# Optimization experiments

Hardware: AMD Instinct MI355X
Metric: run time of the kernel (lower is better)

The kernel has to match this reference:

```python
import jax, jax.numpy as jnp
import numpy as np

D_MODEL = 1024
NUM_HEADS = 16
HEAD_DIM = D_MODEL // NUM_HEADS
LN_EPS = 1e-3  # Keras LayerNormalization default epsilon


def setup_inputs() -> dict:
    key = jax.random.key(0)
    ks = jax.random.split(key, 7)
    s = 1.0 / np.sqrt(D_MODEL)
    return {
        "x": jax.random.normal(ks[0], (2, 2048, D_MODEL), dtype=jnp.float32),
        "Wq": jax.random.normal(ks[1], (D_MODEL, D_MODEL), dtype=jnp.float32) * s,
        "bq": jnp.zeros((D_MODEL,), dtype=jnp.float32),
        "Wk": jax.random.normal(ks[2], (D_MODEL, D_MODEL), dtype=jnp.float32) * s,
        "bk": jnp.zeros((D_MODEL,), dtype=jnp.float32),
        "Wv": jax.random.normal(ks[3], (D_MODEL, D_MODEL), dtype=jnp.float32) * s,
        "bv": jnp.zeros((D_MODEL,), dtype=jnp.float32),
        "ln_gamma": jnp.ones((D_MODEL,), dtype=jnp.float32),
        "ln_beta": jnp.zeros((D_MODEL,), dtype=jnp.float32),
    }


def _split_heads(t):
    # [B, S, D] -> [B, H, S, Dh]; matches tf.split(axis=2)+concat(axis=0) math
    B, S, D = t.shape
    return t.reshape(B, S, NUM_HEADS, HEAD_DIM).transpose(0, 2, 1, 3)


def reference(x, Wq, bq, Wk, bk, Wv, bv, ln_gamma, ln_beta):
    Q = _split_heads(x @ Wq + bq)   # [B,H,S,Dh]
    K = _split_heads(x @ Wk + bk)
    V = _split_heads(x @ Wv + bv)
    scale = 1.0 / jnp.sqrt(jnp.asarray(HEAD_DIM, dtype=x.dtype))
    scores = jnp.einsum("bhqd,bhkd->bhqk", Q, K) * scale
    probs = jax.nn.softmax(scores, axis=-1)  # dropout is identity at inference
    ctx = jnp.einsum("bhqk,bhkd->bhqd", probs, V)
    out = ctx.transpose(0, 2, 1, 3).reshape(x.shape)  # merge heads -> [B,S,D]
    out = out + x  # residual
    mean = jnp.mean(out, axis=-1, keepdims=True)
    var = jnp.mean(jnp.square(out - mean), axis=-1, keepdims=True)
    return (out - mean) * jax.lax.rsqrt(var + LN_EPS) * ln_gamma + ln_beta
```

## Files before the change

### kernel.cpp

```cpp
#include <hip/hip_runtime.h>
#include <stdint.h>

#define D_MODEL 1024
#define SEQ     2048
#define BATCH   2
#define NHEADS  16
#define HDIM    64
#define ROWS    (BATCH*SEQ)

typedef __attribute__((ext_vector_type(8)))  short short8;
typedef __attribute__((ext_vector_type(4)))  float f32x4;
typedef __attribute__((ext_vector_type(16))) float f32x16;
typedef __attribute__((ext_vector_type(4)))  short short4v;

__device__ __forceinline__ unsigned short f2bf(float f){
  union { float f; unsigned int u; } v; v.f = f;
  unsigned int r = v.u + 0x7fffu + ((v.u >> 16) & 1u);
  return (unsigned short)(r >> 16);
}

__device__ __forceinline__ float fast_exp2(float x){
  float r;
  asm("v_exp_f32 %0, %1" : "=v"(r) : "v"(x));
  return r;
}

__device__ __forceinline__ float f3(float a, float b, float c){
  return fmaxf(fmaxf(a,b),c);
}

__device__ __forceinline__ void gload16(const void* g, void* l){
  __builtin_amdgcn_global_load_lds((__attribute__((address_space(1))) void*)(uintptr_t)g,
                                   (__attribute__((address_space(3))) void*)l, 16, 0, 0);
}

__global__ __launch_bounds__(256) void prep(const float* __restrict__ x,
                                            const float* __restrict__ Wq,
                                            const float* __restrict__ Wk,
                                            const float* __restrict__ Wv,
                                            unsigned short* __restrict__ xb,
                                            unsigned short* __restrict__ Wt){
  __shared__ float tile[32][33];
  const int bidx = blockIdx.x;
  if (bidx < 4096){
    const int i = bidx*256 + threadIdx.x;
    float4 v = ((const float4*)x)[i];
    short4v o;
    o[0] = (short)f2bf(v.x); o[1] = (short)f2bf(v.y);
    o[2] = (short)f2bf(v.z); o[3] = (short)f2bf(v.w);
    ((short4v*)xb)[i] = o;
  } else {
    const int wz  = bidx - 4096;
    const int mat = wz >> 10;
    const int idx = wz & 1023;
    const float* W = (mat==0)?Wq:((mat==1)?Wk:Wv);
    unsigned short* dst = Wt + (size_t)mat*1048576;
    const int tx = threadIdx.x & 31, ty = threadIdx.x >> 5;
    const int n0 = (idx & 31)*32, k0 = (idx >> 5)*32;
    #pragma unroll
    for (int j=0;j<32;j+=8)
      tile[ty+j][tx] = W[(size_t)(k0+ty+j)*D_MODEL + n0+tx];
    __syncthreads();
    #pragma unroll
    for (int j=0;j<32;j+=8)
      dst[(size_t)(n0+ty+j)*D_MODEL + k0+tx] = f2bf(tile[tx][ty+j]);
  }
}

__global__ __launch_bounds__(256) void qkv_gemm(
    const unsigned short* __restrict__ xb, const unsigned short* __restrict__ wtb,
    const float* __restrict__ bq, const float* __restrict__ bk, const float* __restrict__ bv,
    unsigned short* __restrict__ qb, unsigned short* __restrict__ kbuf,
    unsigned short* __restrict__ vbuf)
{
  __shared__ unsigned short As[128*32];
  __shared__ unsigned short Bs[128*32];
  const int mat = blockIdx.z;
  const unsigned short* wt = wtb + (size_t)mat*1048576;
  const float* bias = (mat==0)?bq:((mat==1)?bk:bv);
  unsigned short* outp = (mat==0)?qb:((mat==1)?kbuf:vbuf);
  const float osc = (mat==0)?0.18033688011112042f:1.0f;
  const int bm = blockIdx.x, bn = blockIdx.y;
  const int t = threadIdx.x, w = t>>6, lane = t&63;
  const int g = lane>>4, l15 = lane&15;
  const int wm = w>>1, wn = w&1;

  const int srow = (w<<5) + (lane>>2);
  const int scol = (lane&3)*8;

  f32x4 acc[4][4];
  #pragma unroll
  for (int i=0;i<4;++i)
    #pragma unroll
    for (int j=0;j<4;++j) acc[i][j] = (f32x4){0.f,0.f,0.f,0.f};

  for (int kt=0; kt<32; ++kt){
    const int k0 = kt*32;
    #pragma unroll
    for (int j=0;j<2;++j){
      gload16(xb + (size_t)(bm*128 + srow + j*16)*D_MODEL + k0 + scol, &As[(w<<10)+(j<<9)]);
      gload16(wt + (size_t)(bn*128 + srow + j*16)*D_MODEL + k0 + scol, &Bs[(w<<10)+(j<<9)]);
    }
    __syncthreads();
    short8 a[4], b[4];
    #pragma unroll
    for (int mr=0;mr<4;++mr) a[mr] = *(const short8*)&As[(wm*64 + mr*16 + l15)*32 + g*8];
    #pragma unroll
    for (int nr=0;nr<4;++nr) b[nr] = *(const short8*)&Bs[(wn*64 + nr*16 + l15)*32 + g*8];
    #pragma unroll
    for (int mr=0;mr<4;++mr)
      #pragma unroll
      for (int nr=0;nr<4;++nr)
        acc[mr][nr] = __builtin_amdgcn_mfma_f32_16x16x32_bf16(a[mr], b[nr], acc[mr][nr], 0,0,0);
    __syncthreads();
  }
  #pragma unroll
  for (int mr=0;mr<4;++mr){
    const int rowb = bm*128 + wm*64 + mr*16 + g*4;
    #pragma unroll
    for (int nr=0;nr<4;++nr){
      const int col = bn*128 + wn*64 + nr*16 + l15;
      const float bsv = bias[col];
      const int h = col>>6, d = col&63;
      #pragma unroll
      for (int r=0;r<4;++r){
        const int m = rowb + r;
        const int b_ = m>>11, s = m&2047;
        outp[(((size_t)(b_*NHEADS + h))*SEQ + s)*HDIM + d] = f2bf((acc[mr][nr][r] + bsv)*osc);
      }
    }
  }
}

__global__ __launch_bounds__(256) void vtrans(const unsigned short* __restrict__ vb,
                                              unsigned short* __restrict__ vt){
  __shared__ unsigned short tile[64*72];
  const int bh = blockIdx.y;
  const int s0 = blockIdx.x*64;
  const int t = threadIdx.x;
  {
    const int s_loc = t>>2, d0 = (t&3)*16;
    const unsigned short* src = vb + ((size_t)bh*SEQ + s0 + s_loc)*HDIM + d0;
    *(short8*)&tile[s_loc*72 + d0]     = *(const short8*)src;
    *(short8*)&tile[s_loc*72 + d0 + 8] = *(const short8*)(src+8);
  }
  __syncthreads();
  {
    const int d = t>>2, sc = (t&3)*16;
    short8 o0, o1;
    #pragma unroll
    for (int j=0;j<8;++j){
      o0[j] = (short)tile[(sc+j)*72 + d];
      o1[j] = (short)tile[(sc+8+j)*72 + d];
    }
    unsigned short* dst = vt + ((size_t)bh*HDIM + d)*SEQ + s0 + sc;
    *(short8*)dst     = o0;
    *(short8*)(dst+8) = o1;
  }
}

__global__ __launch_bounds__(256, 2) void attn_fwd(
  const unsigned short* __restrict__ Qb, const unsigned short* __restrict__ Kb,
  const unsigned short* __restrict__ Vtb, float* __restrict__ ctx)
{
  __shared__ unsigned short Ks[4][4096];
  __shared__ unsigned short Vs[4][4096];
  const int lin = blockIdx.x;
  const int bh = (lin&7)*4 + (lin>>7);
  const int q0 = ((lin>>3)&15)*128;
  const int t = threadIdx.x, w = t>>6, lane = t&63;
  const int l31 = lane&31, hi = lane>>5;
  const unsigned short* Qh  = Qb  + (size_t)bh*SEQ*HDIM;
  const unsigned short* Kh  = Kb  + (size_t)bh*SEQ*HDIM;
  const unsigned short* Vth = Vtb + (size_t)bh*HDIM*SEQ;

  const int qrow = q0 + w*32 + l31;
  short8 qf[4];
  #pragma unroll
  for (int dht=0;dht<4;++dht)
    qf[dht] = *(const short8*)&Qh[(size_t)qrow*HDIM + dht*16 + hi*8];

  const int srow0 = t>>3,        srow1 = (256+t)>>3;
  const int skk0  = ((t&7)<<3) ^ ((srow0&7)<<3);
  const int skk1  = ((t&7)<<3) ^ ((srow1&7)<<3);
  const int rx    = l31&7;

  float m = 0.f;
  float rsum = 0.f;
  f32x16 o0, o1;
  #pragma unroll
  for (int r=0;r<16;++r){ o0[r]=0.f; o1[r]=0.f; }

#define STAGE(buf, ktile) do {                                                    \
    const int kb_ = (ktile)*64;                                                   \
    gload16(&Kh[(size_t)(kb_ + srow0)*HDIM + skk0], &Ks[buf][(w*64)*8]);          \
    gload16(&Kh[(size_t)(kb_ + srow1)*HDIM + skk1], &Ks[buf][(256 + w*64)*8]);    \
    gload16(&Vth[(size_t)srow0*SEQ + kb_ + skk0],   &Vs[buf][(w*64)*8]);          \
    gload16(&Vth[(size_t)srow1*SEQ + kb_ + skk1],   &Vs[buf][(256 + w*64)*8]);    \
  } while(0)

#define BODY(CUR, KT, HASST, WAITN, FIRST) do {                                   \
    if ((WAITN)==4) asm volatile("s_waitcnt vmcnt(4)" ::: "memory");              \
    else            asm volatile("s_waitcnt vmcnt(0)" ::: "memory");              \
    __builtin_amdgcn_s_barrier();                                                 \
    __builtin_amdgcn_sched_barrier(0);                                            \
    if (HASST) STAGE(((CUR)+2)&3, (KT)+2);                                        \
                                       \
    f32x16 s0, s1;                                                                \
    _Pragma("unroll")                                                             \
    for (int r=0;r<16;++r){ s0[r]=0.f; s1[r]=0.f; }                               \
    __builtin_amdgcn_s_setprio(1);                                                \
    _Pragma("unroll")                                                             \
    for (int dht=0;dht<4;++dht){                                                  \
      short8 kf = *(const short8*)&Ks[CUR][l31*64 + (((dht<<1)|hi) ^ rx)*8];      \
      s0 = __builtin_amdgcn_mfma_f32_32x32x16_bf16(kf, qf[dht], s0, 0,0,0);       \
    }                                                                             \
    _Pragma("unroll")                                                             \
    for (int dht=0;dht<4;++dht){                                                  \
      short8 kf = *(const short8*)&Ks[CUR][(32+l31)*64 + (((dht<<1)|hi) ^ rx)*8]; \
      s1 = __builtin_amdgcn_mfma_f32_32x32x16_bf16(kf, qf[dht], s1, 0,0,0);       \
    }                                                                             \
    __builtin_amdgcn_s_setprio(0);                                                \
    if (FIRST){                                                                   \
      float a0=f3(s0[0],s0[1],s0[2]),  a1=f3(s0[3],s0[4],s0[5]);                  \
      float a2=f3(s0[6],s0[7],s0[8]),  a3=f3(s0[9],s0[10],s0[11]);                \
      float a4=f3(s0[12],s0[13],s0[14]), a5=f3(s0[15],s1[0],s1[1]);               \
      float a6=f3(s1[2],s1[3],s1[4]),  a7=f3(s1[5],s1[6],s1[7]);                  \
      float a8=f3(s1[8],s1[9],s1[10]), a9=f3(s1[11],s1[12],s1[13]);               \
      float a10=fmaxf(s1[14],s1[15]);                                             \
      float rmx = f3(f3(a0,a1,a2), f3(a3,a4,a5), f3(f3(a6,a7,a8), a9, a10));      \
      m = fmaxf(rmx, __shfl_xor(rmx, 32));                                        \
    }                                                                             \
          \
    unsigned int u[8], vv[8];                                                     \
    _Pragma("unroll")                                                             \
    for (int i=0;i<8;++i){                                                        \
      float e0 = fast_exp2(s0[2*i]   - m);                                        \
      float e1 = fast_exp2(s0[2*i+1] - m);                                        \
      float e2 = fast_exp2(s1[2*i]   - m);                                        \
      float e3 = fast_exp2(s1[2*i+1] - m);                                        \
      rsum += (e0+e1)+(e2+e3);                                                    \
      asm("v_cvt_pk_bf16_f32 %0, %1, %2" : "=v"(u[i])  : "v"(e0), "v"(e1));       \
      asm("v_cvt_pk_bf16_f32 %0, %1, %2" : "=v"(vv[i]) : "v"(e2), "v"(e3));       \
    }                                                                             \
    asm("v_permlane32_swap_b32 %0, %1" : "+v"(u[0]),  "+v"(u[2]));                \
    asm("v_permlane32_swap_b32 %0, %1" : "+v"(u[1]),  "+v"(u[3]));                \
    asm("v_permlane32_swap_b32 %0, %1" : "+v"(u[4]),  "+v"(u[6]));                \
    asm("v_permlane32_swap_b32 %0, %1" : "+v"(u[5]),  "+v"(u[7]));                \
    asm("v_permlane32_swap_b32 %0, %1" : "+v"(vv[0]), "+v"(vv[2]));               \
    asm("v_permlane32_swap_b32 %0, %1" : "+v"(vv[1]), "+v"(vv[3]));               \
    asm("v_permlane32_swap_b32 %0, %1" : "+v"(vv[4]), "+v"(vv[6]));               \
    asm("v_permlane32_swap_b32 %0, %1" : "+v"(vv[5]), "+v"(vv[7]));               \
    union U8 { unsigned int wq[4]; short8 s; };                                   \
    short8 pa[4];                                                                 \
    { U8 x; x.wq[0]=u[0];  x.wq[1]=u[1];  x.wq[2]=u[2];  x.wq[3]=u[3];  pa[0]=x.s; } \
    { U8 x; x.wq[0]=u[4];  x.wq[1]=u[5];  x.wq[2]=u[6];  x.wq[3]=u[7];  pa[1]=x.s; } \
    { U8 x; x.wq[0]=vv[0]; x.wq[1]=vv[1]; x.wq[2]=vv[2]; x.wq[3]=vv[3]; pa[2]=x.s; } \
    { U8 x; x.wq[0]=vv[4]; x.wq[1]=vv[5]; x.wq[2]=vv[6]; x.wq[3]=vv[7]; pa[3]=x.s; } \
                                                                    \
    __builtin_amdgcn_s_setprio(1);                                                \
    _Pragma("unroll")                                                             \
    for (int kb=0;kb<4;++kb){                                                     \
      short8 vf0 = *(const short8*)&Vs[CUR][l31*64      + (((kb<<1)|hi) ^ rx)*8]; \
      short8 vf1 = *(const short8*)&Vs[CUR][(32+l31)*64 + (((kb<<1)|hi) ^ rx)*8]; \
      o0 = __builtin_amdgcn_mfma_f32_32x32x16_bf16(pa[kb], vf0, o0, 0,0,0);       \
      o1 = __builtin_amdgcn_mfma_f32_32x32x16_bf16(pa[kb], vf1, o1, 0,0,0);       \
    }                                                                             \
    __builtin_amdgcn_s_setprio(0);                                                \
  } while(0)

  STAGE(0, 0);
  STAGE(1, 1);

  BODY(0, 0, 1, 4, 1);
  BODY(1, 1, 1, 4, 0);
  BODY(2, 2, 1, 4, 0);
  BODY(3, 3, 1, 4, 0);
  for (int kt=4; kt<28; kt+=4){
    BODY(0, kt,   1, 4, 0);
    BODY(1, kt+1, 1, 4, 0);
    BODY(2, kt+2, 1, 4, 0);
    BODY(3, kt+3, 1, 4, 0);
  }
  BODY(0, 28, 1, 4, 0);
  BODY(1, 29, 1, 4, 0);
  BODY(2, 30, 0, 4, 0);
  BODY(3, 31, 0, 0, 0);
#undef BODY
#undef STAGE

  const float rst = rsum + __shfl_xor(rsum, 32);
  const int b_ = bh>>4, h = bh&15;
  #pragma unroll
  for (int r=0;r<16;++r){
    const int cr = (r&3) + ((r>>2)<<3) + (hi<<2);
    const float inv = 1.0f / __shfl(rst, cr);
    const int s = q0 + w*32 + cr;
    float* dst = &ctx[((size_t)(b_*SEQ + s))*D_MODEL + h*64];
    dst[l31]      = o0[r] * inv;
    dst[32 + l31] = o1[r] * inv;
  }
}

__global__ __launch_bounds__(256) void resid_ln(
  const float* __restrict__ ctx, const float* __restrict__ x,
  const float* __restrict__ gamma, const float* __restrict__ beta,
  float* __restrict__ out)
{
  const int row = blockIdx.x, t = threadIdx.x;
  const size_t base = (size_t)row*D_MODEL;
  float4 c  = ((const float4*)(ctx + base))[t];
  float4 xr = ((const float4*)(x   + base))[t];
  float4 v; v.x=c.x+xr.x; v.y=c.y+xr.y; v.z=c.z+xr.z; v.w=c.w+xr.w;
  float s  = v.x+v.y+v.z+v.w;
  float ss = v.x*v.x+v.y*v.y+v.z*v.z+v.w*v.w;
  #pragma unroll
  for (int m=1;m<64;m<<=1){ s += __shfl_xor(s,m); ss += __shfl_xor(ss,m); }
  __shared__ float red[8];
  const int w = t>>6;
  if ((t&63)==0){ red[w] = s; red[4+w] = ss; }
  __syncthreads();
  s  = red[0]+red[1]+red[2]+red[3];
  ss = red[4]+red[5]+red[6]+red[7];
  const float mean = s*(1.f/D_MODEL);
  const float var  = ss*(1.f/D_MODEL) - mean*mean;
  const float rstd = rsqrtf(var + 1e-3f);
  float4 gv = ((const float4*)gamma)[t], bv = ((const float4*)beta)[t];
  float4 ov;
  ov.x=(v.x-mean)*rstd*gv.x+bv.x; ov.y=(v.y-mean)*rstd*gv.y+bv.y;
  ov.z=(v.z-mean)*rstd*gv.z+bv.z; ov.w=(v.w-mean)*rstd*gv.w+bv.w;
  ((float4*)(out + base))[t] = ov;
}

extern "C" void kernel_launch(void* const* d_in, const int* in_sizes, int n_in,
                              void* d_out, int out_size, void* d_ws, size_t ws_size,
                              hipStream_t stream){
  const float* x     = (const float*)d_in[0];
  const float* Wq    = (const float*)d_in[1];
  const float* bq    = (const float*)d_in[2];
  const float* Wk    = (const float*)d_in[3];
  const float* bk    = (const float*)d_in[4];
  const float* Wv    = (const float*)d_in[5];
  const float* bv    = (const float*)d_in[6];
  const float* gamma = (const float*)d_in[7];
  const float* beta  = (const float*)d_in[8];
  float* out = (float*)d_out;

  char* ws = (char*)d_ws;
  unsigned short* xb  = (unsigned short*)(ws);
  unsigned short* wtb = (unsigned short*)(ws + 8388608);
  unsigned short* qb  = (unsigned short*)(ws + 14680064);
  unsigned short* kb  = (unsigned short*)(ws + 23068672);
  unsigned short* vb  = (unsigned short*)(ws + 31457280);
  float* ctx          = (float*)(ws + 39845888);
  unsigned short* vtb = (unsigned short*)(ws);

  hipLaunchKernelGGL(prep,     dim3(7168),              dim3(256), 0, stream,
                     x, Wq, Wk, Wv, xb, wtb);
  hipLaunchKernelGGL(qkv_gemm, dim3(32,8,3),            dim3(256), 0, stream,
                     xb, wtb, bq, bk, bv, qb, kb, vb);
  hipLaunchKernelGGL(vtrans,   dim3(SEQ/64, BATCH*NHEADS), dim3(256), 0, stream, vb, vtb);
  hipLaunchKernelGGL(attn_fwd, dim3(512),               dim3(256), 0, stream, qb, kb, vtb, ctx);
  hipLaunchKernelGGL(resid_ln, dim3(ROWS),              dim3(256), 0, stream, ctx, x, gamma, beta, out);
}
```

Baseline: 108.7 us.

## Double-buffer QKV GEMM loads and simplify attention to two-stage pipeline

The QKV GEMM now double-buffers its LDS tiles, issuing the next k-tile's global-to-LDS loads before computing on the current one, and raises wave priority around the MFMA block. The attention kernel drops from a four-buffer, two-ahead prefetch with explicit vmcnt waits to a two-buffer, one-ahead scheme that syncs with __syncthreads. This aims to hide GEMM load latency and to free LDS in attention for occupancy. The cost is a shallower prefetch in attention, which may expose more latency. The reliance on __syncthreads to drain the async loads also needs to hold.

```diff
diff --git a/kernel.cpp b/kernel.cpp
--- a/kernel.cpp
+++ b/kernel.cpp
@@ -73,8 +73,8 @@
     unsigned short* __restrict__ qb, unsigned short* __restrict__ kbuf,
     unsigned short* __restrict__ vbuf)
 {
-  __shared__ unsigned short As[128*32];
-  __shared__ unsigned short Bs[128*32];
+  __shared__ unsigned short As[2][128*32];
+  __shared__ unsigned short Bs[2][128*32];
   const int mat = blockIdx.z;
   const unsigned short* wt = wtb + (size_t)mat*1048576;
   const float* bias = (mat==0)?bq:((mat==1)?bk:bv);
@@ -94,26 +94,35 @@
     #pragma unroll
     for (int j=0;j<4;++j) acc[i][j] = (f32x4){0.f,0.f,0.f,0.f};
 
+#define QSTAGE(buf, kt) do {                                                       \
+    const int k0 = (kt)*32;                                                        \
+    gload16(xb + (size_t)(bm*128 + srow)*D_MODEL      + k0 + scol, &As[buf][(w<<10)]);        \
+    gload16(xb + (size_t)(bm*128 + srow + 16)*D_MODEL + k0 + scol, &As[buf][(w<<10)+(1<<9)]); \
+    gload16(wt + (size_t)(bn*128 + srow)*D_MODEL      + k0 + scol, &Bs[buf][(w<<10)]);        \
+    gload16(wt + (size_t)(bn*128 + srow + 16)*D_MODEL + k0 + scol, &Bs[buf][(w<<10)+(1<<9)]); \
+  } while(0)
+
+  QSTAGE(0, 0);
+  __syncthreads();
+  int cur = 0;
   for (int kt=0; kt<32; ++kt){
-    const int k0 = kt*32;
-    #pragma unroll
-    for (int j=0;j<2;++j){
-      gload16(xb + (size_t)(bm*128 + srow + j*16)*D_MODEL + k0 + scol, &As[(w<<10)+(j<<9)]);
-      gload16(wt + (size_t)(bn*128 + srow + j*16)*D_MODEL + k0 + scol, &Bs[(w<<10)+(j<<9)]);
-    }
-    __syncthreads();
+    if (kt < 31) QSTAGE(cur^1, kt+1);
     short8 a[4], b[4];
     #pragma unroll
-    for (int mr=0;mr<4;++mr) a[mr] = *(const short8*)&As[(wm*64 + mr*16 + l15)*32 + g*8];
-    #pragma unroll
-    for (int nr=0;nr<4;++nr) b[nr] = *(const short8*)&Bs[(wn*64 + nr*16 + l15)*32 + g*8];
+    for (int mr=0;mr<4;++mr) a[mr] = *(const short8*)&As[cur][(wm*64 + mr*16 + l15)*32 + g*8];
+    #pragma unroll
+    for (int nr=0;nr<4;++nr) b[nr] = *(const short8*)&Bs[cur][(wn*64 + nr*16 + l15)*32 + g*8];
+    __builtin_amdgcn_s_setprio(1);
     #pragma unroll
     for (int mr=0;mr<4;++mr)
       #pragma unroll
       for (int nr=0;nr<4;++nr)
         acc[mr][nr] = __builtin_amdgcn_mfma_f32_16x16x32_bf16(a[mr], b[nr], acc[mr][nr], 0,0,0);
-    __syncthreads();
-  }
+    __builtin_amdgcn_s_setprio(0);
+    if (kt < 31){ __syncthreads(); cur ^= 1; }
+  }
+#undef QSTAGE
+
   #pragma unroll
   for (int mr=0;mr<4;++mr){
     const int rowb = bm*128 + wm*64 + mr*16 + g*4;
@@ -163,8 +172,8 @@
   const unsigned short* __restrict__ Qb, const unsigned short* __restrict__ Kb,
   const unsigned short* __restrict__ Vtb, float* __restrict__ ctx)
 {
-  __shared__ unsigned short Ks[4][4096];
-  __shared__ unsigned short Vs[4][4096];
+  __shared__ unsigned short Ks[2][4096];
+  __shared__ unsigned short Vs[2][4096];
   const int lin = blockIdx.x;
   const int bh = (lin&7)*4 + (lin>>7);
   const int q0 = ((lin>>3)&15)*128;
@@ -199,12 +208,8 @@
     gload16(&Vth[(size_t)srow1*SEQ + kb_ + skk1],   &Vs[buf][(256 + w*64)*8]);    \
   } while(0)
 
-#define BODY(CUR, KT, HASST, WAITN, FIRST) do {                                   \
-    if ((WAITN)==4) asm volatile("s_waitcnt vmcnt(4)" ::: "memory");              \
-    else            asm volatile("s_waitcnt vmcnt(0)" ::: "memory");              \
-    __builtin_amdgcn_s_barrier();                                                 \
-    __builtin_amdgcn_sched_barrier(0);                                            \
-    if (HASST) STAGE(((CUR)+2)&3, (KT)+2);                                        \
+#define BODY(CUR, KT, FIRST) do {                                                 \
+    if ((KT) < 31) STAGE((CUR)^1, (KT)+1);                                        \
                                        \
     f32x16 s0, s1;                                                                \
     _Pragma("unroll")                                                             \
@@ -267,25 +272,18 @@
       o1 = __builtin_amdgcn_mfma_f32_32x32x16_bf16(pa[kb], vf1, o1, 0,0,0);       \
     }                                                                             \
     __builtin_amdgcn_s_setprio(0);                                                \
+    if ((KT) < 31) __syncthreads();                                               \
   } while(0)
 
   STAGE(0, 0);
-  STAGE(1, 1);
-
-  BODY(0, 0, 1, 4, 1);
-  BODY(1, 1, 1, 4, 0);
-  BODY(2, 2, 1, 4, 0);
-  BODY(3, 3, 1, 4, 0);
-  for (int kt=4; kt<28; kt+=4){
-    BODY(0, kt,   1, 4, 0);
-    BODY(1, kt+1, 1, 4, 0);
-    BODY(2, kt+2, 1, 4, 0);
-    BODY(3, kt+3, 1, 4, 0);
-  }
-  BODY(0, 28, 1, 4, 0);
-  BODY(1, 29, 1, 4, 0);
-  BODY(2, 30, 0, 4, 0);
-  BODY(3, 31, 0, 0, 0);
+  __syncthreads();
+
+  BODY(0, 0, 1);
+  BODY(1, 1, 0);
+  for (int kt2=2; kt2<32; kt2+=2){
+    BODY(0, kt2,   0);
+    BODY(1, kt2+1, 0);
+  }
 #undef BODY
 #undef STAGE
 
```

New measurement: 111.1 us. +2.2%, slower.
